# Kernel tuning notes

Hardware: AMD Instinct MI355X
Metric: run time of the kernel (lower is better)

Reference implementation:

```python
import jax, jax.numpy as jnp
import numpy as np

B, S, T, H = 64, 128, 256, 1024
IN = 2 * S  # per-step input: stack(x_t, y_{t-1}) flattened
EMB_IN = 1000


def setup_inputs() -> dict:
    key = jax.random.key(0)
    ks = jax.random.split(key, 13)
    sc = 0.02
    d = {
        "x": jax.random.normal(ks[0], (B, S, T), jnp.float32),
        "subject_id": jax.random.normal(ks[1], (B, EMB_IN), jnp.float32),
        "y": jax.random.normal(ks[2], (B, S, T), jnp.float32),
    }
    gate_names = ["f", "i", "u", "o"]
    for n, kw, kb in zip(gate_names, ks[3:7], ks[7:11]):
        d[f"W_{n}"] = jax.random.normal(kw, (IN + H, H), jnp.float32) * sc
        d[f"b_{n}"] = jax.random.normal(kb, (H,), jnp.float32) * sc
    d["W_init"] = jax.random.normal(ks[11], (EMB_IN, H), jnp.float32) * sc
    d["b_init"] = jax.random.normal(ks[12], (H,), jnp.float32) * sc
    return d


def reference(x, subject_id, y, W_f, b_f, W_i, b_i, W_u, b_u, W_o, b_o, W_init, b_init):
    # embeddings are computed in the torch forward but unused in 'none' mode
    embed = subject_id @ W_init + b_init  # [B, H] (dead in 'none' mode)
    del embed

    # y_prev at step t is y[..., t-1], zeros at t=0
    y_shift = jnp.concatenate([jnp.zeros_like(y[..., :1]), y[..., :-1]], axis=-1)
    # torch.stack((x_t, y_prev), dim=-1).view(B, -1) -> interleaved [B, 2S]
    seq = jnp.stack([x, y_shift], axis=-2)            # [B, S, 2, T]
    seq = jnp.moveaxis(seq, -1, 0).reshape(T, B, IN)  # [T, B, 2S]

    # fuse the 4 gate linears into one GEMM (same math)
    Wg = jnp.concatenate([W_f, W_i, W_u, W_o], axis=1)  # [IN+H, 4H]
    bg = jnp.concatenate([b_f, b_i, b_u, b_o])          # [4H]

    def step(carry, xin):
        h, c = carry
        z = jnp.concatenate([xin, h], axis=1)  # [B, IN+H]
        g = z @ Wg + bg                        # [B, 4H]
        f, i, u, o = jnp.split(g, 4, axis=1)
        c = c * jax.nn.sigmoid(f) + jax.nn.sigmoid(i) * jnp.tanh(u)
        h = jax.nn.sigmoid(o) * jnp.tanh(c)
        return (h, c), h

    h0 = jnp.zeros((B, H), x.dtype)
    (h_T, c_T), hs = jax.lax.scan(step, (h0, h0), seq)
    out = jnp.moveaxis(hs, 0, -1)  # [B, H, T] (torch stacks h along dim=-1)
    return out, c_T
```

## Files before the change

kernel.cpp:

```cpp
#include <hip/hip_runtime.h>
#include <hip/hip_bf16.h>

#define B_ 64
#define T_ 256
#define H_ 1024
#define NB_ 256

typedef __attribute__((ext_vector_type(8))) short short8;
typedef __attribute__((ext_vector_type(4))) float float4_;
typedef unsigned long long u64;

static __device__ __forceinline__ ushort f2bf(float v) {
  __hip_bfloat16 b = __float2bfloat16(v);
  return *reinterpret_cast<ushort*>(&b);
}
static __device__ __forceinline__ float bf2f(ushort u) {
  unsigned int x = ((unsigned int)u) << 16;
  return __builtin_bit_cast(float, x);
}
static __device__ __forceinline__ float sigm(float v) { return 1.0f / (1.0f + __expf(-v)); }
static __device__ __forceinline__ float tanh_fast(float v) {
  float e = __expf(2.0f * v);
  return 1.0f - 2.0f / (e + 1.0f);
}
static __device__ __forceinline__ bool anyS(u64 q) {
  return (q & 0x4000400040004000ull) != 0ull;
}

__global__ __launch_bounds__(256) void build_X(const float* __restrict__ x,
                                               const float* __restrict__ y,
                                               ushort* __restrict__ Xall) {
  __shared__ float xl[128][33];
  __shared__ float yl[128][33];
  int b = blockIdx.x >> 3;
  int t0 = (blockIdx.x & 7) * 32;
  int tid = threadIdx.x;
  for (int it = 0; it < 16; ++it) {
    int idx = it * 256 + tid;
    int s = idx >> 5, tt = idx & 31;
    xl[s][tt] = x[((size_t)b * 128 + s) * T_ + t0 + tt];
    int ty = t0 + tt - 1;
    yl[s][tt] = (ty >= 0) ? y[((size_t)b * 128 + s) * T_ + ty] : 0.0f;
  }
  __syncthreads();
  for (int tt = 0; tt < 32; ++tt) {
    float v = (tid & 1) ? yl[tid >> 1][tt] : xl[tid >> 1][tt];
    Xall[((size_t)(t0 + tt) * B_ + b) * 256 + tid] = f2bf(v);
  }
}

__global__ __launch_bounds__(256) void prep_weights(const float* __restrict__ Wf,
                                                    const float* __restrict__ Wi,
                                                    const float* __restrict__ Wu,
                                                    const float* __restrict__ Wo,
                                                    ushort* __restrict__ Bp) {
  int flat = blockIdx.x * 256 + threadIdx.x;
  int l = flat & 63;
  int r = flat >> 6;
  int u = r % 10;
  int r2 = r / 10;
  int w = r2 & 15;
  int cbl = r2 >> 4;
  int ct = w >> 2, kq = w & 3;
  int kk = (u < 2) ? (2 * kq + u) : (8 + 8 * kq + (u - 2));
  const float* W = (ct == 0) ? Wf : (ct == 1) ? Wi : (ct == 2) ? Wu : Wo;
  int col = cbl * 16 + (l & 15);
  ushort tmp[8];
#pragma unroll
  for (int j = 0; j < 8; ++j) {
    int k = kk * 32 + (l >> 4) * 8 + j;
    tmp[j] = f2bf(W[(size_t)k * H_ + col]);
  }
  *(short8*)(Bp + (size_t)flat * 8) = *(short8*)tmp;
}

template <bool FRESH>
__global__ __launch_bounds__(1024) void lstm_persist(
    const ushort* __restrict__ Xall, const ushort* __restrict__ Bp,
    const float* __restrict__ bfp, const float* __restrict__ bip,
    const float* __restrict__ bup, const float* __restrict__ bop,
    ushort* __restrict__ Hh, float* __restrict__ out,
    unsigned int* __restrict__ flags) {
  __shared__ ushort stg[16][1056];
  __shared__ float gbuf[4][4][16][17];
  __shared__ ushort hbuf[16][16][17];
  const int tid = threadIdx.x;
  const int w = tid >> 6, l = tid & 63;
  const int ct = w >> 2, kq = w & 3;
  const int ar = l & 15, kg = l >> 4;
  const int g = blockIdx.x & 3, cbl = blockIdx.x >> 2;

  short8 bfrag[10];
  {
    const ushort* bp0 = Bp + (((size_t)(cbl * 16 + w) * 10) * 64 + l) * 8;
#pragma unroll
    for (int u = 0; u < 10; ++u) bfrag[u] = *(const short8*)(bp0 + (size_t)u * 512);
  }
#pragma unroll
  for (int u = 0; u < 10; ++u) asm volatile("" : "+v"(bfrag[u]));

  const int b_ep = tid >> 4, hc16 = tid & 15;
  float biasF = 0, biasI = 0, biasU = 0, biasO = 0, creg = 0;
  if (tid < 256) {
    int c = cbl * 16 + hc16;
    biasF = bfp[c]; biasI = bip[c]; biasU = bup[c]; biasO = bop[c];
  }

  for (int t = 0; t < T_; ++t) {
    const ushort* xrow = Xall + ((size_t)t * B_ + 16 * g + ar) * 256 + kg * 8;
    float4_ a0 = {0.f, 0.f, 0.f, 0.f}, a1 = {0.f, 0.f, 0.f, 0.f};
    {
      short8 av0 = *(const short8*)(xrow + (2 * kq) * 32);
      short8 av1 = *(const short8*)(xrow + (2 * kq + 1) * 32);
      a0 = __builtin_amdgcn_mfma_f32_16x16x32_bf16(av0, bfrag[0], a0, 0, 0, 0);
      a1 = __builtin_amdgcn_mfma_f32_16x16x32_bf16(av1, bfrag[1], a1, 0, 0, 0);
    }
    if (t > 0) {
      if (!FRESH) {
        if (tid < 64) {
          unsigned int tgt = (unsigned int)t;
          while (true) {
            unsigned int f0 = __hip_atomic_load(&flags[g * 64 + l], __ATOMIC_RELAXED,
                                                __HIP_MEMORY_SCOPE_AGENT);
            if (__all(f0 >= tgt)) break;
            __builtin_amdgcn_s_sleep(1);
          }
          asm volatile("" ::: "memory");
        }
        __syncthreads();
      }
      {
        const u64* p = (const u64*)(Hh +
            ((size_t)(FRESH ? t : (t & 1)) * 4 + g) * 16384 + (size_t)w * 1024);
        u64 q0, q1, q2, q3;
        if (FRESH) {
          q0 = p[2 * l]; q1 = p[2 * l + 1];
          q2 = p[128 + 2 * l]; q3 = p[129 + 2 * l];
          while (anyS(q0 | q1 | q2 | q3)) {
            __builtin_amdgcn_s_sleep(1);
            q0 = __hip_atomic_load(p + 2 * l, __ATOMIC_RELAXED, __HIP_MEMORY_SCOPE_AGENT);
            q1 = __hip_atomic_load(p + 2 * l + 1, __ATOMIC_RELAXED, __HIP_MEMORY_SCOPE_AGENT);
            q2 = __hip_atomic_load(p + 128 + 2 * l, __ATOMIC_RELAXED, __HIP_MEMORY_SCOPE_AGENT);
            q3 = __hip_atomic_load(p + 129 + 2 * l, __ATOMIC_RELAXED, __HIP_MEMORY_SCOPE_AGENT);
          }
        } else {
          q0 = __hip_atomic_load(p + 2 * l, __ATOMIC_RELAXED, __HIP_MEMORY_SCOPE_AGENT);
          q1 = __hip_atomic_load(p + 2 * l + 1, __ATOMIC_RELAXED, __HIP_MEMORY_SCOPE_AGENT);
          q2 = __hip_atomic_load(p + 128 + 2 * l, __ATOMIC_RELAXED, __HIP_MEMORY_SCOPE_AGENT);
          q3 = __hip_atomic_load(p + 129 + 2 * l, __ATOMIC_RELAXED, __HIP_MEMORY_SCOPE_AGENT);
        }
        union { u64 q[2]; short8 s; } c0, c1;
        c0.q[0] = q0; c0.q[1] = q1; c1.q[0] = q2; c1.q[1] = q3;
        *(short8*)&stg[w][l * 8] = c0.s;
        *(short8*)&stg[w][512 + l * 8] = c1.s;
      }
      __syncthreads();
#pragma unroll
      for (int u = 2; u < 10; ++u) {
        int kk = 8 + 8 * kq + (u - 2);
        short8 av = *(const short8*)&stg[ar][(kk - 8) * 32 + kg * 8];
        if (u & 1) a1 = __builtin_amdgcn_mfma_f32_16x16x32_bf16(av, bfrag[u], a1, 0, 0, 0);
        else       a0 = __builtin_amdgcn_mfma_f32_16x16x32_bf16(av, bfrag[u], a0, 0, 0, 0);
      }
    }
    float4_ acc = a0 + a1;
#pragma unroll
    for (int r = 0; r < 4; ++r) gbuf[ct][kq][kg * 4 + r][ar] = acc[r];
    __syncthreads();
    if (tid < 256) {
      float f  = gbuf[0][0][b_ep][hc16] + gbuf[0][1][b_ep][hc16] +
                 gbuf[0][2][b_ep][hc16] + gbuf[0][3][b_ep][hc16] + biasF;
      float i  = gbuf[1][0][b_ep][hc16] + gbuf[1][1][b_ep][hc16] +
                 gbuf[1][2][b_ep][hc16] + gbuf[1][3][b_ep][hc16] + biasI;
      float uu = gbuf[2][0][b_ep][hc16] + gbuf[2][1][b_ep][hc16] +
                 gbuf[2][2][b_ep][hc16] + gbuf[2][3][b_ep][hc16] + biasU;
      float o  = gbuf[3][0][b_ep][hc16] + gbuf[3][1][b_ep][hc16] +
                 gbuf[3][2][b_ep][hc16] + gbuf[3][3][b_ep][hc16] + biasO;
      creg = fmaf(creg, sigm(f), sigm(i) * tanh_fast(uu));
      float h = sigm(o) * tanh_fast(creg);
      ushort hv = f2bf(h);
      unsigned int hw = hv;
      unsigned int h1 = __shfl_down(hw, 1);
      unsigned int h2 = __shfl_down(hw, 2);
      unsigned int h3 = __shfl_down(hw, 3);
      if ((l & 3) == 0) {
        u64 q = (u64)hw | ((u64)h1 << 16) | ((u64)h2 << 32) | ((u64)h3 << 48);
        u64* dst = (u64*)(Hh +
            ((size_t)(FRESH ? (t + 1) : ((t + 1) & 1)) * 4 + g) * 16384 +
            (size_t)b_ep * 1024 + cbl * 16 + hc16);
        __hip_atomic_store(dst, q, __ATOMIC_RELAXED, __HIP_MEMORY_SCOPE_AGENT);
      }
      hbuf[b_ep][hc16][t & 15] = hv;
      if ((t & 15) == 15) {
        float* orow = out + ((size_t)(16 * g + b_ep) * H_ + cbl * 16 + hc16) * T_ + (t - 15);
#pragma unroll
        for (int tt = 0; tt < 16; tt += 4) {
          float4 v = {bf2f(hbuf[b_ep][hc16][tt]), bf2f(hbuf[b_ep][hc16][tt + 1]),
                      bf2f(hbuf[b_ep][hc16][tt + 2]), bf2f(hbuf[b_ep][hc16][tt + 3])};
          *(float4*)(orow + tt) = v;
        }
      }
    }
    __syncthreads();
    if (!FRESH) {
      asm volatile("s_waitcnt vmcnt(0)" ::: "memory");
      __syncthreads();
      if (tid == 0)
        __hip_atomic_store(&flags[g * 64 + cbl], (unsigned int)(t + 1), __ATOMIC_RELAXED,
                           __HIP_MEMORY_SCOPE_AGENT);
    }
  }
  if (tid < 256)
    out[(size_t)B_ * H_ * T_ + (size_t)(16 * g + b_ep) * H_ + cbl * 16 + hc16] = creg;
}

extern "C" void kernel_launch(void* const* d_in, const int* in_sizes, int n_in,
                              void* d_out, int out_size, void* d_ws, size_t ws_size,
                              hipStream_t stream) {
  const float* x  = (const float*)d_in[0];
  const float* y  = (const float*)d_in[2];
  const float* Wf = (const float*)d_in[3];  const float* bf = (const float*)d_in[4];
  const float* Wi = (const float*)d_in[5];  const float* bi = (const float*)d_in[6];
  const float* Wu = (const float*)d_in[7];  const float* bu = (const float*)d_in[8];
  const float* Wo = (const float*)d_in[9];  const float* bo = (const float*)d_in[10];
  float* out = (float*)d_out;

  char* p = (char*)d_ws;
  ushort* Bp = (ushort*)p;        p += (size_t)64 * 16 * 10 * 64 * 8 * 2;
  ushort* Xall = (ushort*)p;      p += (size_t)T_ * B_ * 256 * 2;
  unsigned int* flags = (unsigned int*)p; p += 4096;
  ushort* Hh = (ushort*)p;
  size_t head = (size_t)(p - (char*)d_ws);
  bool fresh = ws_size >= head + (size_t)(T_ + 1) * 4 * 16384 * 2;

  prep_weights<<<(64 * 16 * 10 * 64) / 256, 256, 0, stream>>>(Wf, Wi, Wu, Wo, Bp);
  build_X<<<B_ * 8, 256, 0, stream>>>(x, y, Xall);
  if (fresh) {
    (void)hipMemsetAsync(Hh, 0xFF, (size_t)(T_ + 1) * 4 * 16384 * 2, stream);
  } else {
    (void)hipMemsetAsync(flags, 0, 4096, stream);
    (void)hipMemsetAsync(Hh, 0, (size_t)2 * 4 * 16384 * 2, stream);
  }

  if (fresh)
    lstm_persist<true><<<NB_, 1024, 0, stream>>>(Xall, Bp, bf, bi, bu, bo, Hh, out, flags);
  else
    lstm_persist<false><<<NB_, 1024, 0, stream>>>(Xall, Bp, bf, bi, bu, bo, Hh, out, flags);
}
```

Measured before the change: 714.7 us.

## Repartition LSTM blocks into 8 batch groups by 32 hidden columns

Changes how the persistent LSTM kernel splits work. Blocks now own 8 batch rows by 32 hidden columns (8 batch groups × 32 column blocks) instead of 16 rows by 16 columns. Each wave holds 20 weight fragments covering half of K for one 16-column tile, so each block reads only half as much of the previous h from global memory per step, and the epilogue sums just two partial sums per gate. The catch is that half the MFMA rows are padding (8 real rows in a 16-row tile), register pressure is higher, and each block waits on more producers, 32 flags instead of 64 per group but with a different fan-in. A volatile store is also added before the atomic h store.

Result: slower. 979.2 us (+37.0%).

```diff
diff --git a/kernel.cpp b/kernel.cpp
--- a/kernel.cpp
+++ b/kernel.cpp
@@ -5,6 +5,8 @@
 #define T_ 256
 #define H_ 1024
 #define NB_ 256
+#define NG_ 8
+#define NCB_ 32
 
 typedef __attribute__((ext_vector_type(8))) short short8;
 typedef __attribute__((ext_vector_type(4))) float float4_;
@@ -57,14 +59,15 @@
   int flat = blockIdx.x * 256 + threadIdx.x;
   int l = flat & 63;
   int r = flat >> 6;
-  int u = r % 10;
-  int r2 = r / 10;
+  int u = r % 20;
+  int r2 = r / 20;
   int w = r2 & 15;
   int cbl = r2 >> 4;
-  int ct = w >> 2, kq = w & 3;
-  int kk = (u < 2) ? (2 * kq + u) : (8 + 8 * kq + (u - 2));
-  const float* W = (ct == 0) ? Wf : (ct == 1) ? Wi : (ct == 2) ? Wu : Wo;
-  int col = cbl * 16 + (l & 15);
+  int ntile = w >> 1, khalf = w & 1;
+  int kk = 2 * u + khalf;
+  int gt = ntile >> 1, hn = ntile & 1;
+  const float* W = (gt == 0) ? Wf : (gt == 1) ? Wi : (gt == 2) ? Wu : Wo;
+  int col = cbl * 32 + hn * 16 + (l & 15);
   ushort tmp[8];
 #pragma unroll
   for (int j = 0; j < 8; ++j) {
@@ -81,46 +84,47 @@
     const float* __restrict__ bup, const float* __restrict__ bop,
     ushort* __restrict__ Hh, float* __restrict__ out,
     unsigned int* __restrict__ flags) {
-  __shared__ ushort stg[16][1056];
-  __shared__ float gbuf[4][4][16][17];
-  __shared__ ushort hbuf[16][16][17];
+  __shared__ ushort stg[8][1040];
+  __shared__ float gbuf[8][2][16][17];
+  __shared__ ushort hbuf[8][32][17];
   const int tid = threadIdx.x;
   const int w = tid >> 6, l = tid & 63;
-  const int ct = w >> 2, kq = w & 3;
+  const int ntile = w >> 1, khalf = w & 1;
   const int ar = l & 15, kg = l >> 4;
-  const int g = blockIdx.x & 3, cbl = blockIdx.x >> 2;
-
-  short8 bfrag[10];
+  const int br = ar & 7;
+  const int g = blockIdx.x & 7, cbl = blockIdx.x >> 3;
+
+  short8 bfrag[20];
   {
-    const ushort* bp0 = Bp + (((size_t)(cbl * 16 + w) * 10) * 64 + l) * 8;
-#pragma unroll
-    for (int u = 0; u < 10; ++u) bfrag[u] = *(const short8*)(bp0 + (size_t)u * 512);
-  }
-#pragma unroll
-  for (int u = 0; u < 10; ++u) asm volatile("" : "+v"(bfrag[u]));
-
-  const int b_ep = tid >> 4, hc16 = tid & 15;
+    const ushort* bp0 = Bp + (((size_t)(cbl * 16 + w) * 20) * 64 + l) * 8;
+#pragma unroll
+    for (int u = 0; u < 20; ++u) bfrag[u] = *(const short8*)(bp0 + (size_t)u * 512);
+  }
+#pragma unroll
+  for (int u = 0; u < 20; ++u) asm volatile("" : "+v"(bfrag[u]));
+
+  const int b_ep = tid >> 5, j_ep = tid & 31;
   float biasF = 0, biasI = 0, biasU = 0, biasO = 0, creg = 0;
   if (tid < 256) {
-    int c = cbl * 16 + hc16;
+    int c = cbl * 32 + j_ep;
     biasF = bfp[c]; biasI = bip[c]; biasU = bup[c]; biasO = bop[c];
   }
 
   for (int t = 0; t < T_; ++t) {
-    const ushort* xrow = Xall + ((size_t)t * B_ + 16 * g + ar) * 256 + kg * 8;
+    const ushort* xrow = Xall + ((size_t)t * B_ + 8 * g + br) * 256 + kg * 8;
     float4_ a0 = {0.f, 0.f, 0.f, 0.f}, a1 = {0.f, 0.f, 0.f, 0.f};
-    {
-      short8 av0 = *(const short8*)(xrow + (2 * kq) * 32);
-      short8 av1 = *(const short8*)(xrow + (2 * kq + 1) * 32);
-      a0 = __builtin_amdgcn_mfma_f32_16x16x32_bf16(av0, bfrag[0], a0, 0, 0, 0);
-      a1 = __builtin_amdgcn_mfma_f32_16x16x32_bf16(av1, bfrag[1], a1, 0, 0, 0);
+#pragma unroll
+    for (int u = 0; u < 4; ++u) {
+      short8 av = *(const short8*)(xrow + (2 * u + khalf) * 32);
+      if (u & 1) a1 = __builtin_amdgcn_mfma_f32_16x16x32_bf16(av, bfrag[u], a1, 0, 0, 0);
+      else       a0 = __builtin_amdgcn_mfma_f32_16x16x32_bf16(av, bfrag[u], a0, 0, 0, 0);
     }
     if (t > 0) {
       if (!FRESH) {
-        if (tid < 64) {
+        if (tid < 32) {
           unsigned int tgt = (unsigned int)t;
           while (true) {
-            unsigned int f0 = __hip_atomic_load(&flags[g * 64 + l], __ATOMIC_RELAXED,
+            unsigned int f0 = __hip_atomic_load(&flags[g * 32 + l], __ATOMIC_RELAXED,
                                                 __HIP_MEMORY_SCOPE_AGENT);
             if (__all(f0 >= tgt)) break;
             __builtin_amdgcn_s_sleep(1);
@@ -130,52 +134,44 @@
         __syncthreads();
       }
       {
-        const u64* p = (const u64*)(Hh +
-            ((size_t)(FRESH ? t : (t & 1)) * 4 + g) * 16384 + (size_t)w * 1024);
-        u64 q0, q1, q2, q3;
+        const size_t slot = ((size_t)(FRESH ? t : (t & 1)) * NG_ + g) * 8192;
+        const int sr = w >> 1, sh = (w & 1) * 512;
+        const u64* p = (const u64*)(Hh + slot + (size_t)sr * 1024 + sh + l * 8);
+        u64 q0, q1;
         if (FRESH) {
-          q0 = p[2 * l]; q1 = p[2 * l + 1];
-          q2 = p[128 + 2 * l]; q3 = p[129 + 2 * l];
-          while (anyS(q0 | q1 | q2 | q3)) {
+          q0 = p[0]; q1 = p[1];
+          while (anyS(q0 | q1)) {
             __builtin_amdgcn_s_sleep(1);
-            q0 = __hip_atomic_load(p + 2 * l, __ATOMIC_RELAXED, __HIP_MEMORY_SCOPE_AGENT);
-            q1 = __hip_atomic_load(p + 2 * l + 1, __ATOMIC_RELAXED, __HIP_MEMORY_SCOPE_AGENT);
-            q2 = __hip_atomic_load(p + 128 + 2 * l, __ATOMIC_RELAXED, __HIP_MEMORY_SCOPE_AGENT);
-            q3 = __hip_atomic_load(p + 129 + 2 * l, __ATOMIC_RELAXED, __HIP_MEMORY_SCOPE_AGENT);
+            q0 = __hip_atomic_load(p, __ATOMIC_RELAXED, __HIP_MEMORY_SCOPE_AGENT);
+            q1 = __hip_atomic_load(p + 1, __ATOMIC_RELAXED, __HIP_MEMORY_SCOPE_AGENT);
           }
         } else {
-          q0 = __hip_atomic_load(p + 2 * l, __ATOMIC_RELAXED, __HIP_MEMORY_SCOPE_AGENT);
-          q1 = __hip_atomic_load(p + 2 * l + 1, __ATOMIC_RELAXED, __HIP_MEMORY_SCOPE_AGENT);
-          q2 = __hip_atomic_load(p + 128 + 2 * l, __ATOMIC_RELAXED, __HIP_MEMORY_SCOPE_AGENT);
-          q3 = __hip_atomic_load(p + 129 + 2 * l, __ATOMIC_RELAXED, __HIP_MEMORY_SCOPE_AGENT);
+          q0 = __hip_atomic_load(p, __ATOMIC_RELAXED, __HIP_MEMORY_SCOPE_AGENT);
+          q1 = __hip_atomic_load(p + 1, __ATOMIC_RELAXED, __HIP_MEMORY_SCOPE_AGENT);
         }
-        union { u64 q[2]; short8 s; } c0, c1;
-        c0.q[0] = q0; c0.q[1] = q1; c1.q[0] = q2; c1.q[1] = q3;
-        *(short8*)&stg[w][l * 8] = c0.s;
-        *(short8*)&stg[w][512 + l * 8] = c1.s;
+        union { u64 q[2]; short8 s; } cv;
+        cv.q[0] = q0; cv.q[1] = q1;
+        *(short8*)&stg[sr][sh + l * 8] = cv.s;
       }
       __syncthreads();
 #pragma unroll
-      for (int u = 2; u < 10; ++u) {
-        int kk = 8 + 8 * kq + (u - 2);
-        short8 av = *(const short8*)&stg[ar][(kk - 8) * 32 + kg * 8];
+      for (int u = 4; u < 20; ++u) {
+        int kk = 2 * u + khalf;
+        short8 av = *(const short8*)&stg[br][(kk - 8) * 32 + kg * 8];
         if (u & 1) a1 = __builtin_amdgcn_mfma_f32_16x16x32_bf16(av, bfrag[u], a1, 0, 0, 0);
         else       a0 = __builtin_amdgcn_mfma_f32_16x16x32_bf16(av, bfrag[u], a0, 0, 0, 0);
       }
     }
     float4_ acc = a0 + a1;
 #pragma unroll
-    for (int r = 0; r < 4; ++r) gbuf[ct][kq][kg * 4 + r][ar] = acc[r];
+    for (int r = 0; r < 4; ++r) gbuf[ntile][khalf][kg * 4 + r][ar] = acc[r];
     __syncthreads();
     if (tid < 256) {
-      float f  = gbuf[0][0][b_ep][hc16] + gbuf[0][1][b_ep][hc16] +
-                 gbuf[0][2][b_ep][hc16] + gbuf[0][3][b_ep][hc16] + biasF;
-      float i  = gbuf[1][0][b_ep][hc16] + gbuf[1][1][b_ep][hc16] +
-                 gbuf[1][2][b_ep][hc16] + gbuf[1][3][b_ep][hc16] + biasI;
-      float uu = gbuf[2][0][b_ep][hc16] + gbuf[2][1][b_ep][hc16] +
-                 gbuf[2][2][b_ep][hc16] + gbuf[2][3][b_ep][hc16] + biasU;
-      float o  = gbuf[3][0][b_ep][hc16] + gbuf[3][1][b_ep][hc16] +
-                 gbuf[3][2][b_ep][hc16] + gbuf[3][3][b_ep][hc16] + biasO;
+      int nt = j_ep >> 4, c16 = j_ep & 15;
+      float f  = gbuf[nt][0][b_ep][c16] + gbuf[nt][1][b_ep][c16] + biasF;
+      float i  = gbuf[2 + nt][0][b_ep][c16] + gbuf[2 + nt][1][b_ep][c16] + biasI;
+      float uu = gbuf[4 + nt][0][b_ep][c16] + gbuf[4 + nt][1][b_ep][c16] + biasU;
+      float o  = gbuf[6 + nt][0][b_ep][c16] + gbuf[6 + nt][1][b_ep][c16] + biasO;
       creg = fmaf(creg, sigm(f), sigm(i) * tanh_fast(uu));
       float h = sigm(o) * tanh_fast(creg);
       ushort hv = f2bf(h);
@@ -186,17 +182,18 @@
       if ((l & 3) == 0) {
         u64 q = (u64)hw | ((u64)h1 << 16) | ((u64)h2 << 32) | ((u64)h3 << 48);
         u64* dst = (u64*)(Hh +
-            ((size_t)(FRESH ? (t + 1) : ((t + 1) & 1)) * 4 + g) * 16384 +
-            (size_t)b_ep * 1024 + cbl * 16 + hc16);
+            ((size_t)(FRESH ? (t + 1) : ((t + 1) & 1)) * NG_ + g) * 8192 +
+            (size_t)b_ep * 1024 + cbl * 32 + j_ep);
+        *(volatile u64*)dst = q;
         __hip_atomic_store(dst, q, __ATOMIC_RELAXED, __HIP_MEMORY_SCOPE_AGENT);
       }
-      hbuf[b_ep][hc16][t & 15] = hv;
+      hbuf[b_ep][j_ep][t & 15] = hv;
       if ((t & 15) == 15) {
-        float* orow = out + ((size_t)(16 * g + b_ep) * H_ + cbl * 16 + hc16) * T_ + (t - 15);
+        float* orow = out + ((size_t)(8 * g + b_ep) * H_ + cbl * 32 + j_ep) * T_ + (t - 15);
 #pragma unroll
         for (int tt = 0; tt < 16; tt += 4) {
-          float4 v = {bf2f(hbuf[b_ep][hc16][tt]), bf2f(hbuf[b_ep][hc16][tt + 1]),
-                      bf2f(hbuf[b_ep][hc16][tt + 2]), bf2f(hbuf[b_ep][hc16][tt + 3])};
+          float4 v = {bf2f(hbuf[b_ep][j_ep][tt]), bf2f(hbuf[b_ep][j_ep][tt + 1]),
+                      bf2f(hbuf[b_ep][j_ep][tt + 2]), bf2f(hbuf[b_ep][j_ep][tt + 3])};
           *(float4*)(orow + tt) = v;
         }
       }
@@ -206,12 +203,12 @@
       asm volatile("s_waitcnt vmcnt(0)" ::: "memory");
       __syncthreads();
       if (tid == 0)
-        __hip_atomic_store(&flags[g * 64 + cbl], (unsigned int)(t + 1), __ATOMIC_RELAXED,
+        __hip_atomic_store(&flags[g * 32 + cbl], (unsigned int)(t + 1), __ATOMIC_RELAXED,
                            __HIP_MEMORY_SCOPE_AGENT);
     }
   }
   if (tid < 256)
-    out[(size_t)B_ * H_ * T_ + (size_t)(16 * g + b_ep) * H_ + cbl * 16 + hc16] = creg;
+    out[(size_t)B_ * H_ * T_ + (size_t)(8 * g + b_ep) * H_ + cbl * 32 + j_ep] = creg;
 }
 
 extern "C" void kernel_launch(void* const* d_in, const int* in_sizes, int n_in,
@@ -226,20 +223,20 @@
   float* out = (float*)d_out;
 
   char* p = (char*)d_ws;
-  ushort* Bp = (ushort*)p;        p += (size_t)64 * 16 * 10 * 64 * 8 * 2;
+  ushort* Bp = (ushort*)p;        p += (size_t)NCB_ * 16 * 20 * 64 * 8 * 2;
   ushort* Xall = (ushort*)p;      p += (size_t)T_ * B_ * 256 * 2;
   unsigned int* flags = (unsigned int*)p; p += 4096;
   ushort* Hh = (ushort*)p;
   size_t head = (size_t)(p - (char*)d_ws);
-  bool fresh = ws_size >= head + (size_t)(T_ + 1) * 4 * 16384 * 2;
-
-  prep_weights<<<(64 * 16 * 10 * 64) / 256, 256, 0, stream>>>(Wf, Wi, Wu, Wo, Bp);
+  bool fresh = ws_size >= head + (size_t)(T_ + 1) * NG_ * 8192 * 2;
+
+  prep_weights<<<(NCB_ * 16 * 20 * 64) / 256, 256, 0, stream>>>(Wf, Wi, Wu, Wo, Bp);
   build_X<<<B_ * 8, 256, 0, stream>>>(x, y, Xall);
   if (fresh) {
-    (void)hipMemsetAsync(Hh, 0xFF, (size_t)(T_ + 1) * 4 * 16384 * 2, stream);
+    (void)hipMemsetAsync(Hh, 0xFF, (size_t)(T_ + 1) * NG_ * 8192 * 2, stream);
   } else {
     (void)hipMemsetAsync(flags, 0, 4096, stream);
-    (void)hipMemsetAsync(Hh, 0, (size_t)2 * 4 * 16384 * 2, stream);
+    (void)hipMemsetAsync(Hh, 0, (size_t)2 * NG_ * 8192 * 2, stream);
   }
 
   if (fresh)
```

## Halve LSTM block to 8 waves with 2-way K split and doubled per-wave fragments

Applied to the files above, without the earlier changes.

Switches the persistent LSTM kernel from 16 waves (4 gates × 4 K-quarters) to 8 waves (4 gates × 2 K-halves). Each wave now keeps 20 weight fragments in registers, runs twice as many MFMAs per step, and loads two rows of the h staging buffer. This reduces the cross-wave reduction in shared memory and the per-block thread count, which may lower barrier and epilogue overhead. In exchange each wave does more serial MFMA work per step and holds more VGPRs.

Result: faster. 683.1 us (-4.4%).

```diff
diff --git a/kernel.cpp b/kernel.cpp
--- a/kernel.cpp
+++ b/kernel.cpp
@@ -57,12 +57,12 @@
   int flat = blockIdx.x * 256 + threadIdx.x;
   int l = flat & 63;
   int r = flat >> 6;
-  int u = r % 10;
-  int r2 = r / 10;
-  int w = r2 & 15;
-  int cbl = r2 >> 4;
-  int ct = w >> 2, kq = w & 3;
-  int kk = (u < 2) ? (2 * kq + u) : (8 + 8 * kq + (u - 2));
+  int u = r % 20;
+  int r2 = r / 20;
+  int w = r2 & 7;
+  int cbl = r2 >> 3;
+  int ct = w >> 1, kq = w & 1;
+  int kk = (u < 4) ? (4 * kq + u) : (8 + 16 * kq + (u - 4));
   const float* W = (ct == 0) ? Wf : (ct == 1) ? Wi : (ct == 2) ? Wu : Wo;
   int col = cbl * 16 + (l & 15);
   ushort tmp[8];
@@ -75,29 +75,29 @@
 }
 
 template <bool FRESH>
-__global__ __launch_bounds__(1024) void lstm_persist(
+__global__ __launch_bounds__(512) void lstm_persist(
     const ushort* __restrict__ Xall, const ushort* __restrict__ Bp,
     const float* __restrict__ bfp, const float* __restrict__ bip,
     const float* __restrict__ bup, const float* __restrict__ bop,
     ushort* __restrict__ Hh, float* __restrict__ out,
     unsigned int* __restrict__ flags) {
   __shared__ ushort stg[16][1056];
-  __shared__ float gbuf[4][4][16][17];
+  __shared__ float gbuf[4][2][16][17];
   __shared__ ushort hbuf[16][16][17];
   const int tid = threadIdx.x;
   const int w = tid >> 6, l = tid & 63;
-  const int ct = w >> 2, kq = w & 3;
+  const int ct = w >> 1, kq = w & 1;
   const int ar = l & 15, kg = l >> 4;
   const int g = blockIdx.x & 3, cbl = blockIdx.x >> 2;
 
-  short8 bfrag[10];
+  short8 bfrag[20];
   {
-    const ushort* bp0 = Bp + (((size_t)(cbl * 16 + w) * 10) * 64 + l) * 8;
-#pragma unroll
-    for (int u = 0; u < 10; ++u) bfrag[u] = *(const short8*)(bp0 + (size_t)u * 512);
-  }
-#pragma unroll
-  for (int u = 0; u < 10; ++u) asm volatile("" : "+v"(bfrag[u]));
+    const ushort* bp0 = Bp + (((size_t)(cbl * 8 + w) * 20) * 64 + l) * 8;
+#pragma unroll
+    for (int u = 0; u < 20; ++u) bfrag[u] = *(const short8*)(bp0 + (size_t)u * 512);
+  }
+#pragma unroll
+  for (int u = 0; u < 20; ++u) asm volatile("" : "+v"(bfrag[u]));
 
   const int b_ep = tid >> 4, hc16 = tid & 15;
   float biasF = 0, biasI = 0, biasU = 0, biasO = 0, creg = 0;
@@ -109,11 +109,11 @@
   for (int t = 0; t < T_; ++t) {
     const ushort* xrow = Xall + ((size_t)t * B_ + 16 * g + ar) * 256 + kg * 8;
     float4_ a0 = {0.f, 0.f, 0.f, 0.f}, a1 = {0.f, 0.f, 0.f, 0.f};
-    {
-      short8 av0 = *(const short8*)(xrow + (2 * kq) * 32);
-      short8 av1 = *(const short8*)(xrow + (2 * kq + 1) * 32);
-      a0 = __builtin_amdgcn_mfma_f32_16x16x32_bf16(av0, bfrag[0], a0, 0, 0, 0);
-      a1 = __builtin_amdgcn_mfma_f32_16x16x32_bf16(av1, bfrag[1], a1, 0, 0, 0);
+#pragma unroll
+    for (int u = 0; u < 4; ++u) {
+      short8 av = *(const short8*)(xrow + (4 * kq + u) * 32);
+      if (u & 1) a1 = __builtin_amdgcn_mfma_f32_16x16x32_bf16(av, bfrag[u], a1, 0, 0, 0);
+      else       a0 = __builtin_amdgcn_mfma_f32_16x16x32_bf16(av, bfrag[u], a0, 0, 0, 0);
     }
     if (t > 0) {
       if (!FRESH) {
@@ -130,34 +130,48 @@
         __syncthreads();
       }
       {
-        const u64* p = (const u64*)(Hh +
-            ((size_t)(FRESH ? t : (t & 1)) * 4 + g) * 16384 + (size_t)w * 1024);
-        u64 q0, q1, q2, q3;
+        const ushort* slot = Hh + ((size_t)(FRESH ? t : (t & 1)) * 4 + g) * 16384;
+        const u64* pA = (const u64*)(slot + (size_t)w * 1024);
+        const u64* pB = (const u64*)(slot + (size_t)(w + 8) * 1024);
+        u64 q0, q1, q2, q3, q4, q5, q6, q7;
         if (FRESH) {
-          q0 = p[2 * l]; q1 = p[2 * l + 1];
-          q2 = p[128 + 2 * l]; q3 = p[129 + 2 * l];
-          while (anyS(q0 | q1 | q2 | q3)) {
+          q0 = pA[2 * l];       q1 = pA[2 * l + 1];
+          q2 = pA[128 + 2 * l]; q3 = pA[129 + 2 * l];
+          q4 = pB[2 * l];       q5 = pB[2 * l + 1];
+          q6 = pB[128 + 2 * l]; q7 = pB[129 + 2 * l];
+          while (anyS(q0 | q1 | q2 | q3 | q4 | q5 | q6 | q7)) {
             __builtin_amdgcn_s_sleep(1);
-            q0 = __hip_atomic_load(p + 2 * l, __ATOMIC_RELAXED, __HIP_MEMORY_SCOPE_AGENT);
-            q1 = __hip_atomic_load(p + 2 * l + 1, __ATOMIC_RELAXED, __HIP_MEMORY_SCOPE_AGENT);
-            q2 = __hip_atomic_load(p + 128 + 2 * l, __ATOMIC_RELAXED, __HIP_MEMORY_SCOPE_AGENT);
-            q3 = __hip_atomic_load(p + 129 + 2 * l, __ATOMIC_RELAXED, __HIP_MEMORY_SCOPE_AGENT);
+            q0 = __hip_atomic_load(pA + 2 * l, __ATOMIC_RELAXED, __HIP_MEMORY_SCOPE_AGENT);
+            q1 = __hip_atomic_load(pA + 2 * l + 1, __ATOMIC_RELAXED, __HIP_MEMORY_SCOPE_AGENT);
+            q2 = __hip_atomic_load(pA + 128 + 2 * l, __ATOMIC_RELAXED, __HIP_MEMORY_SCOPE_AGENT);
+            q3 = __hip_atomic_load(pA + 129 + 2 * l, __ATOMIC_RELAXED, __HIP_MEMORY_SCOPE_AGENT);
+            q4 = __hip_atomic_load(pB + 2 * l, __ATOMIC_RELAXED, __HIP_MEMORY_SCOPE_AGENT);
+            q5 = __hip_atomic_load(pB + 2 * l + 1, __ATOMIC_RELAXED, __HIP_MEMORY_SCOPE_AGENT);
+            q6 = __hip_atomic_load(pB + 128 + 2 * l, __ATOMIC_RELAXED, __HIP_MEMORY_SCOPE_AGENT);
+            q7 = __hip_atomic_load(pB + 129 + 2 * l, __ATOMIC_RELAXED, __HIP_MEMORY_SCOPE_AGENT);
           }
         } else {
-          q0 = __hip_atomic_load(p + 2 * l, __ATOMIC_RELAXED, __HIP_MEMORY_SCOPE_AGENT);
-          q1 = __hip_atomic_load(p + 2 * l + 1, __ATOMIC_RELAXED, __HIP_MEMORY_SCOPE_AGENT);
-          q2 = __hip_atomic_load(p + 128 + 2 * l, __ATOMIC_RELAXED, __HIP_MEMORY_SCOPE_AGENT);
-          q3 = __hip_atomic_load(p + 129 + 2 * l, __ATOMIC_RELAXED, __HIP_MEMORY_SCOPE_AGENT);
+          q0 = __hip_atomic_load(pA + 2 * l, __ATOMIC_RELAXED, __HIP_MEMORY_SCOPE_AGENT);
+          q1 = __hip_atomic_load(pA + 2 * l + 1, __ATOMIC_RELAXED, __HIP_MEMORY_SCOPE_AGENT);
+          q2 = __hip_atomic_load(pA + 128 + 2 * l, __ATOMIC_RELAXED, __HIP_MEMORY_SCOPE_AGENT);
+          q3 = __hip_atomic_load(pA + 129 + 2 * l, __ATOMIC_RELAXED, __HIP_MEMORY_SCOPE_AGENT);
+          q4 = __hip_atomic_load(pB + 2 * l, __ATOMIC_RELAXED, __HIP_MEMORY_SCOPE_AGENT);
+          q5 = __hip_atomic_load(pB + 2 * l + 1, __ATOMIC_RELAXED, __HIP_MEMORY_SCOPE_AGENT);
+          q6 = __hip_atomic_load(pB + 128 + 2 * l, __ATOMIC_RELAXED, __HIP_MEMORY_SCOPE_AGENT);
+          q7 = __hip_atomic_load(pB + 129 + 2 * l, __ATOMIC_RELAXED, __HIP_MEMORY_SCOPE_AGENT);
         }
-        union { u64 q[2]; short8 s; } c0, c1;
+        union { u64 q[2]; short8 s; } c0, c1, c2, c3;
         c0.q[0] = q0; c0.q[1] = q1; c1.q[0] = q2; c1.q[1] = q3;
+        c2.q[0] = q4; c2.q[1] = q5; c3.q[0] = q6; c3.q[1] = q7;
         *(short8*)&stg[w][l * 8] = c0.s;
         *(short8*)&stg[w][512 + l * 8] = c1.s;
+        *(short8*)&stg[w + 8][l * 8] = c2.s;
+        *(short8*)&stg[w + 8][512 + l * 8] = c3.s;
       }
       __syncthreads();
 #pragma unroll
-      for (int u = 2; u < 10; ++u) {
-        int kk = 8 + 8 * kq + (u - 2);
+      for (int u = 4; u < 20; ++u) {
+        int kk = 8 + 16 * kq + (u - 4);
         short8 av = *(const short8*)&stg[ar][(kk - 8) * 32 + kg * 8];
         if (u & 1) a1 = __builtin_amdgcn_mfma_f32_16x16x32_bf16(av, bfrag[u], a1, 0, 0, 0);
         else       a0 = __builtin_amdgcn_mfma_f32_16x16x32_bf16(av, bfrag[u], a0, 0, 0, 0);
@@ -168,14 +182,10 @@
     for (int r = 0; r < 4; ++r) gbuf[ct][kq][kg * 4 + r][ar] = acc[r];
     __syncthreads();
     if (tid < 256) {
-      float f  = gbuf[0][0][b_ep][hc16] + gbuf[0][1][b_ep][hc16] +
-                 gbuf[0][2][b_ep][hc16] + gbuf[0][3][b_ep][hc16] + biasF;
-      float i  = gbuf[1][0][b_ep][hc16] + gbuf[1][1][b_ep][hc16] +
-                 gbuf[1][2][b_ep][hc16] + gbuf[1][3][b_ep][hc16] + biasI;
-      float uu = gbuf[2][0][b_ep][hc16] + gbuf[2][1][b_ep][hc16] +
-                 gbuf[2][2][b_ep][hc16] + gbuf[2][3][b_ep][hc16] + biasU;
-      float o  = gbuf[3][0][b_ep][hc16] + gbuf[3][1][b_ep][hc16] +
-                 gbuf[3][2][b_ep][hc16] + gbuf[3][3][b_ep][hc16] + biasO;
+      float f  = gbuf[0][0][b_ep][hc16] + gbuf[0][1][b_ep][hc16] + biasF;
+      float i  = gbuf[1][0][b_ep][hc16] + gbuf[1][1][b_ep][hc16] + biasI;
+      float uu = gbuf[2][0][b_ep][hc16] + gbuf[2][1][b_ep][hc16] + biasU;
+      float o  = gbuf[3][0][b_ep][hc16] + gbuf[3][1][b_ep][hc16] + biasO;
       creg = fmaf(creg, sigm(f), sigm(i) * tanh_fast(uu));
       float h = sigm(o) * tanh_fast(creg);
       ushort hv = f2bf(h);
@@ -226,14 +236,14 @@
   float* out = (float*)d_out;
 
   char* p = (char*)d_ws;
-  ushort* Bp = (ushort*)p;        p += (size_t)64 * 16 * 10 * 64 * 8 * 2;
+  ushort* Bp = (ushort*)p;        p += (size_t)64 * 8 * 20 * 64 * 8 * 2;
   ushort* Xall = (ushort*)p;      p += (size_t)T_ * B_ * 256 * 2;
   unsigned int* flags = (unsigned int*)p; p += 4096;
   ushort* Hh = (ushort*)p;
   size_t head = (size_t)(p - (char*)d_ws);
   bool fresh = ws_size >= head + (size_t)(T_ + 1) * 4 * 16384 * 2;
 
-  prep_weights<<<(64 * 16 * 10 * 64) / 256, 256, 0, stream>>>(Wf, Wi, Wu, Wo, Bp);
+  prep_weights<<<(64 * 8 * 20 * 64) / 256, 256, 0, stream>>>(Wf, Wi, Wu, Wo, Bp);
   build_X<<<B_ * 8, 256, 0, stream>>>(x, y, Xall);
   if (fresh) {
     (void)hipMemsetAsync(Hh, 0xFF, (size_t)(T_ + 1) * 4 * 16384 * 2, stream);
@@ -243,7 +253,7 @@
   }
 
   if (fresh)
-    lstm_persist<true><<<NB_, 1024, 0, stream>>>(Xall, Bp, bf, bi, bu, bo, Hh, out, flags);
+    lstm_persist<true><<<NB_, 512, 0, stream>>>(Xall, Bp, bf, bi, bu, bo, Hh, out, flags);
   else
-    lstm_persist<false><<<NB_, 1024, 0, stream>>>(Xall, Bp, bf, bi, bu, bo, Hh, out, flags);
-}
+    lstm_persist<false><<<NB_, 512, 0, stream>>>(Xall, Bp, bf, bi, bu, bo, Hh, out, flags);
+}
```

## Give each wave full K reduction and interleaved gate columns, drop cross-wave reduction

Applied to the files above, without the earlier changes.

Restructures the persistent LSTM kernel from 16 waves that split K and gates into 4 waves per block. Each wave now holds all 40 K-chunks of weights in registers, for columns interleaved across the four gates. Gate values are gathered with lane shuffles instead of a shared-memory cross-wave reduction, which removes a barrier and the gbuf traffic. H staging is double-buffered and XOR-swizzled to avoid LDS bank conflicts. The cost is much higher register pressure (40 short8 fragments per lane) and fewer threads loading h each step.

Measured after the change: 818.3 us. 14.5% more time.

```diff
diff --git a/kernel.cpp b/kernel.cpp
--- a/kernel.cpp
+++ b/kernel.cpp
@@ -5,6 +5,7 @@
 #define T_ 256
 #define H_ 1024
 #define NB_ 256
+#define NKK_ 40
 
 typedef __attribute__((ext_vector_type(8))) short short8;
 typedef __attribute__((ext_vector_type(4))) float float4_;
@@ -25,6 +26,11 @@
 }
 static __device__ __forceinline__ bool anyS(u64 q) {
   return (q & 0x4000400040004000ull) != 0ull;
+}
+static __device__ __forceinline__ float pick4(int r, float v0, float v1, float v2, float v3) {
+  float x = (r == 1) ? v1 : v0;
+  float y = (r == 3) ? v3 : v2;
+  return (r & 2) ? y : x;
 }
 
 __global__ __launch_bounds__(256) void build_X(const float* __restrict__ x,
@@ -56,64 +62,65 @@
                                                     ushort* __restrict__ Bp) {
   int flat = blockIdx.x * 256 + threadIdx.x;
   int l = flat & 63;
-  int r = flat >> 6;
-  int u = r % 10;
-  int r2 = r / 10;
-  int w = r2 & 15;
-  int cbl = r2 >> 4;
-  int ct = w >> 2, kq = w & 3;
-  int kk = (u < 2) ? (2 * kq + u) : (8 + 8 * kq + (u - 2));
-  const float* W = (ct == 0) ? Wf : (ct == 1) ? Wi : (ct == 2) ? Wu : Wo;
-  int col = cbl * 16 + (l & 15);
+  int g2 = flat >> 6;
+  int kk = g2 % NKK_;
+  int nb = g2 / NKK_;
+  int q = l & 15, kg = l >> 4;
+  int gt = q >> 2, m = q & 3;
+  const float* W = (gt == 0) ? Wf : (gt == 1) ? Wi : (gt == 2) ? Wu : Wo;
+  int col = nb * 4 + m;
   ushort tmp[8];
 #pragma unroll
   for (int j = 0; j < 8; ++j) {
-    int k = kk * 32 + (l >> 4) * 8 + j;
+    int k = kk * 32 + kg * 8 + j;
     tmp[j] = f2bf(W[(size_t)k * H_ + col]);
   }
   *(short8*)(Bp + (size_t)flat * 8) = *(short8*)tmp;
 }
 
 template <bool FRESH>
-__global__ __launch_bounds__(1024) void lstm_persist(
+__global__ __launch_bounds__(256) void lstm_persist(
     const ushort* __restrict__ Xall, const ushort* __restrict__ Bp,
     const float* __restrict__ bfp, const float* __restrict__ bip,
     const float* __restrict__ bup, const float* __restrict__ bop,
     ushort* __restrict__ Hh, float* __restrict__ out,
     unsigned int* __restrict__ flags) {
-  __shared__ ushort stg[16][1056];
-  __shared__ float gbuf[4][4][16][17];
-  __shared__ ushort hbuf[16][16][17];
+  __shared__ ushort stg[2][16][1024];
+  __shared__ ushort hbuf[4][16][4][17];
   const int tid = threadIdx.x;
-  const int w = tid >> 6, l = tid & 63;
-  const int ct = w >> 2, kq = w & 3;
+  const int wv = tid >> 6, l = tid & 63;
   const int ar = l & 15, kg = l >> 4;
   const int g = blockIdx.x & 3, cbl = blockIdx.x >> 2;
-
-  short8 bfrag[10];
+  const int nb4 = cbl * 4 + wv;
+
+  short8 bfrag[NKK_];
   {
-    const ushort* bp0 = Bp + (((size_t)(cbl * 16 + w) * 10) * 64 + l) * 8;
-#pragma unroll
-    for (int u = 0; u < 10; ++u) bfrag[u] = *(const short8*)(bp0 + (size_t)u * 512);
-  }
-#pragma unroll
-  for (int u = 0; u < 10; ++u) asm volatile("" : "+v"(bfrag[u]));
-
-  const int b_ep = tid >> 4, hc16 = tid & 15;
-  float biasF = 0, biasI = 0, biasU = 0, biasO = 0, creg = 0;
-  if (tid < 256) {
-    int c = cbl * 16 + hc16;
-    biasF = bfp[c]; biasI = bip[c]; biasU = bup[c]; biasO = bop[c];
-  }
+    const ushort* bp0 = Bp + (((size_t)nb4 * NKK_) * 64 + l) * 8;
+#pragma unroll
+    for (int u = 0; u < NKK_; ++u) bfrag[u] = *(const short8*)(bp0 + (size_t)u * 512);
+  }
+#pragma unroll
+  for (int u = 0; u < NKK_; ++u) asm volatile("" : "+v"(bfrag[u]));
+
+  const int rho = (l >> 2) & 3, m = l & 3, hi = l >> 4;
+  const int row_o = hi * 4 + rho;
+  const int hcol = cbl * 16 + wv * 4 + m;
+  const float biasF = bfp[hcol], biasI = bip[hcol];
+  const float biasU = bup[hcol], biasO = bop[hcol];
+  float creg = 0.0f;
+  const int srow = tid >> 4, sc = tid & 15;
 
   for (int t = 0; t < T_; ++t) {
+    const int par = t & 1;
     const ushort* xrow = Xall + ((size_t)t * B_ + 16 * g + ar) * 256 + kg * 8;
-    float4_ a0 = {0.f, 0.f, 0.f, 0.f}, a1 = {0.f, 0.f, 0.f, 0.f};
-    {
-      short8 av0 = *(const short8*)(xrow + (2 * kq) * 32);
-      short8 av1 = *(const short8*)(xrow + (2 * kq + 1) * 32);
-      a0 = __builtin_amdgcn_mfma_f32_16x16x32_bf16(av0, bfrag[0], a0, 0, 0, 0);
-      a1 = __builtin_amdgcn_mfma_f32_16x16x32_bf16(av1, bfrag[1], a1, 0, 0, 0);
+    float4_ a0 = {0, 0, 0, 0}, a1 = {0, 0, 0, 0}, a2 = {0, 0, 0, 0}, a3 = {0, 0, 0, 0};
+#pragma unroll
+    for (int u = 0; u < 8; ++u) {
+      short8 av = *(const short8*)(xrow + u * 32);
+      if ((u & 3) == 0) a0 = __builtin_amdgcn_mfma_f32_16x16x32_bf16(av, bfrag[u], a0, 0, 0, 0);
+      else if ((u & 3) == 1) a1 = __builtin_amdgcn_mfma_f32_16x16x32_bf16(av, bfrag[u], a1, 0, 0, 0);
+      else if ((u & 3) == 2) a2 = __builtin_amdgcn_mfma_f32_16x16x32_bf16(av, bfrag[u], a2, 0, 0, 0);
+      else a3 = __builtin_amdgcn_mfma_f32_16x16x32_bf16(av, bfrag[u], a3, 0, 0, 0);
     }
     if (t > 0) {
       if (!FRESH) {
@@ -130,78 +137,97 @@
         __syncthreads();
       }
       {
-        const u64* p = (const u64*)(Hh +
-            ((size_t)(FRESH ? t : (t & 1)) * 4 + g) * 16384 + (size_t)w * 1024);
-        u64 q0, q1, q2, q3;
+        const ushort* slotp = Hh + ((size_t)(FRESH ? t : par) * 4 + g) * 16384;
+        const u64* pr = (const u64*)(slotp + (size_t)srow * 1024);
+        u64 q[16];
         if (FRESH) {
-          q0 = p[2 * l]; q1 = p[2 * l + 1];
-          q2 = p[128 + 2 * l]; q3 = p[129 + 2 * l];
-          while (anyS(q0 | q1 | q2 | q3)) {
+#pragma unroll
+          for (int i = 0; i < 8; ++i) {
+            q[2 * i] = pr[sc * 2 + i * 32];
+            q[2 * i + 1] = pr[sc * 2 + 1 + i * 32];
+          }
+          u64 acc_or = 0;
+#pragma unroll
+          for (int i = 0; i < 16; ++i) acc_or |= q[i];
+          while (anyS(acc_or)) {
             __builtin_amdgcn_s_sleep(1);
-            q0 = __hip_atomic_load(p + 2 * l, __ATOMIC_RELAXED, __HIP_MEMORY_SCOPE_AGENT);
-            q1 = __hip_atomic_load(p + 2 * l + 1, __ATOMIC_RELAXED, __HIP_MEMORY_SCOPE_AGENT);
-            q2 = __hip_atomic_load(p + 128 + 2 * l, __ATOMIC_RELAXED, __HIP_MEMORY_SCOPE_AGENT);
-            q3 = __hip_atomic_load(p + 129 + 2 * l, __ATOMIC_RELAXED, __HIP_MEMORY_SCOPE_AGENT);
+#pragma unroll
+            for (int i = 0; i < 8; ++i) {
+              q[2 * i] = __hip_atomic_load(pr + sc * 2 + i * 32, __ATOMIC_RELAXED,
+                                           __HIP_MEMORY_SCOPE_AGENT);
+              q[2 * i + 1] = __hip_atomic_load(pr + sc * 2 + 1 + i * 32, __ATOMIC_RELAXED,
+                                               __HIP_MEMORY_SCOPE_AGENT);
+            }
+            acc_or = 0;
+#pragma unroll
+            for (int i = 0; i < 16; ++i) acc_or |= q[i];
           }
         } else {
-          q0 = __hip_atomic_load(p + 2 * l, __ATOMIC_RELAXED, __HIP_MEMORY_SCOPE_AGENT);
-          q1 = __hip_atomic_load(p + 2 * l + 1, __ATOMIC_RELAXED, __HIP_MEMORY_SCOPE_AGENT);
-          q2 = __hip_atomic_load(p + 128 + 2 * l, __ATOMIC_RELAXED, __HIP_MEMORY_SCOPE_AGENT);
-          q3 = __hip_atomic_load(p + 129 + 2 * l, __ATOMIC_RELAXED, __HIP_MEMORY_SCOPE_AGENT);
-        }
-        union { u64 q[2]; short8 s; } c0, c1;
-        c0.q[0] = q0; c0.q[1] = q1; c1.q[0] = q2; c1.q[1] = q3;
-        *(short8*)&stg[w][l * 8] = c0.s;
-        *(short8*)&stg[w][512 + l * 8] = c1.s;
+#pragma unroll
+          for (int i = 0; i < 8; ++i) {
+            q[2 * i] = __hip_atomic_load(pr + sc * 2 + i * 32, __ATOMIC_RELAXED,
+                                         __HIP_MEMORY_SCOPE_AGENT);
+            q[2 * i + 1] = __hip_atomic_load(pr + sc * 2 + 1 + i * 32, __ATOMIC_RELAXED,
+                                             __HIP_MEMORY_SCOPE_AGENT);
+          }
+        }
+#pragma unroll
+        for (int i = 0; i < 8; ++i) {
+          union { u64 qq[2]; short8 s; } cv;
+          cv.qq[0] = q[2 * i]; cv.qq[1] = q[2 * i + 1];
+          *(short8*)&stg[par][srow][(sc * 8 + i * 128) ^ ((srow & 7) << 3)] = cv.s;
+        }
       }
       __syncthreads();
 #pragma unroll
-      for (int u = 2; u < 10; ++u) {
-        int kk = 8 + 8 * kq + (u - 2);
-        short8 av = *(const short8*)&stg[ar][(kk - 8) * 32 + kg * 8];
-        if (u & 1) a1 = __builtin_amdgcn_mfma_f32_16x16x32_bf16(av, bfrag[u], a1, 0, 0, 0);
-        else       a0 = __builtin_amdgcn_mfma_f32_16x16x32_bf16(av, bfrag[u], a0, 0, 0, 0);
-      }
-    }
-    float4_ acc = a0 + a1;
-#pragma unroll
-    for (int r = 0; r < 4; ++r) gbuf[ct][kq][kg * 4 + r][ar] = acc[r];
-    __syncthreads();
-    if (tid < 256) {
-      float f  = gbuf[0][0][b_ep][hc16] + gbuf[0][1][b_ep][hc16] +
-                 gbuf[0][2][b_ep][hc16] + gbuf[0][3][b_ep][hc16] + biasF;
-      float i  = gbuf[1][0][b_ep][hc16] + gbuf[1][1][b_ep][hc16] +
-                 gbuf[1][2][b_ep][hc16] + gbuf[1][3][b_ep][hc16] + biasI;
-      float uu = gbuf[2][0][b_ep][hc16] + gbuf[2][1][b_ep][hc16] +
-                 gbuf[2][2][b_ep][hc16] + gbuf[2][3][b_ep][hc16] + biasU;
-      float o  = gbuf[3][0][b_ep][hc16] + gbuf[3][1][b_ep][hc16] +
-                 gbuf[3][2][b_ep][hc16] + gbuf[3][3][b_ep][hc16] + biasO;
-      creg = fmaf(creg, sigm(f), sigm(i) * tanh_fast(uu));
-      float h = sigm(o) * tanh_fast(creg);
+      for (int u = 8; u < NKK_; ++u) {
+        short8 av = *(const short8*)&stg[par][ar][((u - 8) * 32 + kg * 8) ^ ((ar & 7) << 3)];
+        if ((u & 3) == 0) a0 = __builtin_amdgcn_mfma_f32_16x16x32_bf16(av, bfrag[u], a0, 0, 0, 0);
+        else if ((u & 3) == 1) a1 = __builtin_amdgcn_mfma_f32_16x16x32_bf16(av, bfrag[u], a1, 0, 0, 0);
+        else if ((u & 3) == 2) a2 = __builtin_amdgcn_mfma_f32_16x16x32_bf16(av, bfrag[u], a2, 0, 0, 0);
+        else a3 = __builtin_amdgcn_mfma_f32_16x16x32_bf16(av, bfrag[u], a3, 0, 0, 0);
+      }
+    }
+    float4_ accv = (a0 + a1) + (a2 + a3);
+    {
+      const int sb = (l & 48) | (l & 3);
+      float S00 = __shfl(accv[0], sb),      S01 = __shfl(accv[1], sb);
+      float S02 = __shfl(accv[2], sb),      S03 = __shfl(accv[3], sb);
+      float S10 = __shfl(accv[0], sb + 4),  S11 = __shfl(accv[1], sb + 4);
+      float S12 = __shfl(accv[2], sb + 4),  S13 = __shfl(accv[3], sb + 4);
+      float S20 = __shfl(accv[0], sb + 8),  S21 = __shfl(accv[1], sb + 8);
+      float S22 = __shfl(accv[2], sb + 8),  S23 = __shfl(accv[3], sb + 8);
+      float S30 = __shfl(accv[0], sb + 12), S31 = __shfl(accv[1], sb + 12);
+      float S32 = __shfl(accv[2], sb + 12), S33 = __shfl(accv[3], sb + 12);
+      float F = pick4(rho, S00, S01, S02, S03) + biasF;
+      float I = pick4(rho, S10, S11, S12, S13) + biasI;
+      float U = pick4(rho, S20, S21, S22, S23) + biasU;
+      float O = pick4(rho, S30, S31, S32, S33) + biasO;
+      creg = fmaf(creg, sigm(F), sigm(I) * tanh_fast(U));
+      float h = sigm(O) * tanh_fast(creg);
       ushort hv = f2bf(h);
       unsigned int hw = hv;
       unsigned int h1 = __shfl_down(hw, 1);
       unsigned int h2 = __shfl_down(hw, 2);
       unsigned int h3 = __shfl_down(hw, 3);
       if ((l & 3) == 0) {
-        u64 q = (u64)hw | ((u64)h1 << 16) | ((u64)h2 << 32) | ((u64)h3 << 48);
+        u64 qv = (u64)hw | ((u64)h1 << 16) | ((u64)h2 << 32) | ((u64)h3 << 48);
         u64* dst = (u64*)(Hh +
             ((size_t)(FRESH ? (t + 1) : ((t + 1) & 1)) * 4 + g) * 16384 +
-            (size_t)b_ep * 1024 + cbl * 16 + hc16);
-        __hip_atomic_store(dst, q, __ATOMIC_RELAXED, __HIP_MEMORY_SCOPE_AGENT);
-      }
-      hbuf[b_ep][hc16][t & 15] = hv;
+            (size_t)row_o * 1024 + cbl * 16 + wv * 4);
+        __hip_atomic_store(dst, qv, __ATOMIC_RELAXED, __HIP_MEMORY_SCOPE_AGENT);
+      }
+      hbuf[wv][row_o][m][t & 15] = hv;
       if ((t & 15) == 15) {
-        float* orow = out + ((size_t)(16 * g + b_ep) * H_ + cbl * 16 + hc16) * T_ + (t - 15);
+        float* orow = out + ((size_t)(16 * g + row_o) * H_ + hcol) * T_ + (t - 15);
 #pragma unroll
         for (int tt = 0; tt < 16; tt += 4) {
-          float4 v = {bf2f(hbuf[b_ep][hc16][tt]), bf2f(hbuf[b_ep][hc16][tt + 1]),
-                      bf2f(hbuf[b_ep][hc16][tt + 2]), bf2f(hbuf[b_ep][hc16][tt + 3])};
+          float4 v = {bf2f(hbuf[wv][row_o][m][tt]), bf2f(hbuf[wv][row_o][m][tt + 1]),
+                      bf2f(hbuf[wv][row_o][m][tt + 2]), bf2f(hbuf[wv][row_o][m][tt + 3])};
           *(float4*)(orow + tt) = v;
         }
       }
     }
-    __syncthreads();
     if (!FRESH) {
       asm volatile("s_waitcnt vmcnt(0)" ::: "memory");
       __syncthreads();
@@ -210,8 +236,7 @@
                            __HIP_MEMORY_SCOPE_AGENT);
     }
   }
-  if (tid < 256)
-    out[(size_t)B_ * H_ * T_ + (size_t)(16 * g + b_ep) * H_ + cbl * 16 + hc16] = creg;
+  out[(size_t)B_ * H_ * T_ + (size_t)(16 * g + row_o) * H_ + hcol] = creg;
 }
 
 extern "C" void kernel_launch(void* const* d_in, const int* in_sizes, int n_in,
@@ -226,14 +251,14 @@
   float* out = (float*)d_out;
 
   char* p = (char*)d_ws;
-  ushort* Bp = (ushort*)p;        p += (size_t)64 * 16 * 10 * 64 * 8 * 2;
+  ushort* Bp = (ushort*)p;        p += (size_t)256 * NKK_ * 64 * 8 * 2;
   ushort* Xall = (ushort*)p;      p += (size_t)T_ * B_ * 256 * 2;
   unsigned int* flags = (unsigned int*)p; p += 4096;
   ushort* Hh = (ushort*)p;
   size_t head = (size_t)(p - (char*)d_ws);
   bool fresh = ws_size >= head + (size_t)(T_ + 1) * 4 * 16384 * 2;
 
-  prep_weights<<<(64 * 16 * 10 * 64) / 256, 256, 0, stream>>>(Wf, Wi, Wu, Wo, Bp);
+  prep_weights<<<(256 * NKK_ * 64) / 256, 256, 0, stream>>>(Wf, Wi, Wu, Wo, Bp);
   build_X<<<B_ * 8, 256, 0, stream>>>(x, y, Xall);
   if (fresh) {
     (void)hipMemsetAsync(Hh, 0xFF, (size_t)(T_ + 1) * 4 * 16384 * 2, stream);
@@ -243,7 +268,7 @@
   }
 
   if (fresh)
-    lstm_persist<true><<<NB_, 1024, 0, stream>>>(Xall, Bp, bf, bi, bu, bo, Hh, out, flags);
+    lstm_persist<true><<<NB_, 256, 0, stream>>>(Xall, Bp, bf, bi, bu, bo, Hh, out, flags);
   else
-    lstm_persist<false><<<NB_, 1024, 0, stream>>>(Xall, Bp, bf, bi, bu, bo, Hh, out, flags);
-}
+    lstm_persist<false><<<NB_, 256, 0, stream>>>(Xall, Bp, bf, bi, bu, bo, Hh, out, flags);
+}
```
